# Performance work log

Measured on AMD Instinct MI355X. Metric: run time of the kernel, lower is better.

## Reference

```python
import jax, jax.numpy as jnp
import numpy as np

B, IN_DIM, HID, OUT_DIM, K = 16384, 400, 24, 4096, 64


def setup_inputs() -> dict:
    key = jax.random.key(0)
    ks = jax.random.split(key, 20)
    bnd = 1.0 / np.sqrt(IN_DIM)

    def factorized_eps(k, shape):
        # sign(x)*sqrt(|x|) of small gaussian noise, outer-product factorized
        if len(shape) == 2:
            ko, ki = jax.random.split(k)
            eo = jax.random.normal(ko, (shape[0],)) * 0.001
            ei = jax.random.normal(ki, (shape[1],)) * 0.001
            f = lambda v: jnp.sign(v) * jnp.sqrt(jnp.abs(v))
            return jnp.outer(f(eo), f(ei))
        e = jax.random.normal(k, shape) * 0.001
        return jnp.sign(e) * jnp.sqrt(jnp.abs(e))

    sig2 = 0.5 / np.sqrt(HID)
    sig3 = 0.5 / np.sqrt(OUT_DIM)
    bnd24 = 1.0 / np.sqrt(HID)
    return {
        "x": jax.random.normal(ks[0], (B, IN_DIM), dtype=jnp.float32),
        "possible_moves": jax.random.randint(ks[1], (B, K), 0, OUT_DIM),
        "W1": jax.random.uniform(ks[2], (HID, IN_DIM), minval=-bnd, maxval=bnd),
        "b1": jax.random.uniform(ks[3], (HID,), minval=-bnd, maxval=bnd),
        "mu_w2": jax.random.uniform(ks[4], (HID, HID), minval=-bnd24, maxval=bnd24),
        "mu_b2": jax.random.uniform(ks[5], (HID,), minval=-bnd24, maxval=bnd24),
        "sigma_w2": jnp.full((HID, HID), sig2, dtype=jnp.float32),
        "sigma_b2": jnp.full((HID,), sig2, dtype=jnp.float32),
        "eps_w2": factorized_eps(ks[6], (HID, HID)),
        "eps_b2": factorized_eps(ks[7], (HID,)),
        "mu_w3": jax.random.uniform(ks[8], (OUT_DIM, HID), minval=-bnd24, maxval=bnd24),
        "mu_b3": jax.random.uniform(ks[9], (OUT_DIM,), minval=-bnd24, maxval=bnd24),
        "sigma_w3": jnp.full((OUT_DIM, HID), sig3, dtype=jnp.float32),
        "sigma_b3": jnp.full((OUT_DIM,), sig3, dtype=jnp.float32),
        "eps_w3": factorized_eps(ks[10], (OUT_DIM, HID)),
        "eps_b3": factorized_eps(ks[11], (OUT_DIM,)),
    }


def reference(x, possible_moves, W1, b1, mu_w2, mu_b2, sigma_w2, sigma_b2,
              eps_w2, eps_b2, mu_w3, mu_b3, sigma_w3, sigma_b3, eps_w3, eps_b3):
    h = jax.nn.relu(x @ W1.T + b1)
    w2 = mu_w2 + sigma_w2 * eps_w2
    h = jax.nn.relu(h @ w2.T + (mu_b2 + sigma_b2 * eps_b2))
    w3 = mu_w3 + sigma_w3 * eps_w3
    logits = h @ w3.T + (mu_b3 + sigma_b3 * eps_b3)  # [B, OUT_DIM]
    # scatter 1.0 at legal-move indices per row (vectorized LegalSoftmax)
    rows = jnp.arange(logits.shape[0])[:, None]
    mask = jnp.zeros(logits.shape, logits.dtype).at[rows, possible_moves].set(1.0)
    filtered = logits * mask
    return jnp.where(filtered == 0, -jnp.inf, filtered)
```

## Files before the change

### kernel.cpp

```cpp
#include <hip/hip_runtime.h>
#include <math.h>

#define BATCH 16384
#define IN_DIM 400
#define HID 24
#define OUT_DIM 4096
#define KMOV 64

#define SENT_BITS 0xFF7F0000u

#define WS_W3   0
#define WS_B3   (WS_W3 + OUT_DIM * HID)
#define WS_W2   (WS_B3 + OUT_DIM)
#define WS_B2   (WS_W2 + HID * HID)
#define WS_NEED ((size_t)(WS_B2 + HID) * sizeof(float))

__global__ __launch_bounds__(256) void precompute_folds(
    const float* __restrict__ mu_w2, const float* __restrict__ mu_b2,
    const float* __restrict__ sigma_w2, const float* __restrict__ sigma_b2,
    const float* __restrict__ eps_w2, const float* __restrict__ eps_b2,
    const float* __restrict__ mu_w3, const float* __restrict__ sigma_w3,
    const float* __restrict__ eps_w3, const float* __restrict__ mu_b3,
    const float* __restrict__ sigma_b3, const float* __restrict__ eps_b3,
    float* __restrict__ ws) {
    const int stride = gridDim.x * blockDim.x;
    const int g = blockIdx.x * blockDim.x + threadIdx.x;
    for (int i = g; i < OUT_DIM * HID; i += stride)
        ws[WS_W3 + i] = mu_w3[i] + sigma_w3[i] * eps_w3[i];
    for (int i = g; i < OUT_DIM; i += stride)
        ws[WS_B3 + i] = mu_b3[i] + sigma_b3[i] * eps_b3[i];
    for (int i = g; i < HID * HID; i += stride)
        ws[WS_W2 + i] = mu_w2[i] + sigma_w2[i] * eps_w2[i];
    for (int i = g; i < HID; i += stride)
        ws[WS_B2 + i] = mu_b2[i] + sigma_b2[i] * eps_b2[i];
}

__global__ __launch_bounds__(256) void noisy_onepass(
    const float* __restrict__ x, const int* __restrict__ moves,
    const float* __restrict__ W1, const float* __restrict__ b1,
    const float* __restrict__ ws, float* __restrict__ out) {
    __shared__ float rowbuf[OUT_DIM];
    __shared__ float w2s[HID * HID];
    __shared__ float b2s[HID];
    __shared__ float h1s[HID];
    __shared__ float h2s[HID];

    const int tid = threadIdx.x;
    const int lane = tid & 63;
    const int wave = tid >> 6;
    const int row = blockIdx.x;
    const float SENT = __uint_as_float(SENT_BITS);

    const float4 n4 = make_float4(SENT, SENT, SENT, SENT);
    float4* rb4 = (float4*)rowbuf;
#pragma unroll
    for (int i = 0; i < 4; ++i) rb4[i * 256 + tid] = n4;

    int idx = 0;
    if (tid < KMOV) idx = moves[(size_t)row * KMOV + tid];

    for (int i = tid; i < HID * HID; i += 256) w2s[i] = ws[WS_W2 + i];
    if (tid < HID) b2s[tid] = ws[WS_B2 + tid];

    {
        const float4* xv = (const float4*)(x + (size_t)row * IN_DIM);
        const float4* w1v = (const float4*)W1;
        float4 xa = xv[lane];
        float4 xb = make_float4(0.f, 0.f, 0.f, 0.f);
        const bool hasB = (lane < IN_DIM / 4 - 64);
        if (hasB) xb = xv[64 + lane];

#pragma unroll
        for (int t = 0; t < 6; ++t) {
            const int u = wave * 6 + t;
            const float4* wrow = w1v + u * (IN_DIM / 4);
            float4 wa = wrow[lane];
            float acc = xa.x * wa.x + xa.y * wa.y + xa.z * wa.z + xa.w * wa.w;
            if (hasB) {
                float4 wb = wrow[64 + lane];
                acc += xb.x * wb.x + xb.y * wb.y + xb.z * wb.z + xb.w * wb.w;
            }
            acc += __shfl_xor(acc, 32);
            acc += __shfl_xor(acc, 16);
            acc += __shfl_xor(acc, 8);
            acc += __shfl_xor(acc, 4);
            acc += __shfl_xor(acc, 2);
            acc += __shfl_xor(acc, 1);
            if (lane == 0) h1s[u] = fmaxf(acc + b1[u], 0.f);
        }
    }
    __syncthreads();

    if (tid < HID) {
        float acc = b2s[tid];
#pragma unroll
        for (int j = 0; j < HID; ++j) acc += h1s[j] * w2s[tid * HID + j];
        h2s[tid] = fmaxf(acc, 0.f);
    }
    __syncthreads();

    if (tid < KMOV) {
        float acc = ws[WS_B3 + idx];
        const float4* wr = (const float4*)(ws + WS_W3 + idx * HID);
#pragma unroll
        for (int q = 0; q < 6; ++q) {
            float4 w4 = wr[q];
            acc += h2s[q * 4 + 0] * w4.x + h2s[q * 4 + 1] * w4.y +
                   h2s[q * 4 + 2] * w4.z + h2s[q * 4 + 3] * w4.w;
        }
        rowbuf[idx] = (acc != 0.f) ? acc : SENT;
    }
    __syncthreads();

    float4* orow = (float4*)(out + (size_t)row * OUT_DIM);
#pragma unroll
    for (int i = 0; i < 4; ++i) orow[i * 256 + tid] = rb4[i * 256 + tid];
}

__global__ __launch_bounds__(256) void noisy_fused_fly(
    const float* __restrict__ x, const int* __restrict__ moves,
    const float* __restrict__ W1, const float* __restrict__ b1,
    const float* __restrict__ mu_w2, const float* __restrict__ mu_b2,
    const float* __restrict__ sigma_w2, const float* __restrict__ sigma_b2,
    const float* __restrict__ eps_w2, const float* __restrict__ eps_b2,
    const float* __restrict__ mu_w3, const float* __restrict__ mu_b3,
    const float* __restrict__ sigma_w3, const float* __restrict__ sigma_b3,
    const float* __restrict__ eps_w3, const float* __restrict__ eps_b3,
    float* __restrict__ out) {
    __shared__ float rowbuf[OUT_DIM];
    __shared__ float w2s[HID * HID];
    __shared__ float b2s[HID];
    __shared__ float h1s[HID];
    __shared__ float h2s[HID];

    const int tid = threadIdx.x;
    const int lane = tid & 63;
    const int wave = tid >> 6;
    const int row = blockIdx.x;
    const float SENT = __uint_as_float(SENT_BITS);

    const float4 n4 = make_float4(SENT, SENT, SENT, SENT);
    float4* rb4 = (float4*)rowbuf;
#pragma unroll
    for (int i = 0; i < 4; ++i) rb4[i * 256 + tid] = n4;

    int idx = 0;
    if (tid < KMOV) idx = moves[(size_t)row * KMOV + tid];

    for (int i = tid; i < HID * HID; i += 256)
        w2s[i] = mu_w2[i] + sigma_w2[i] * eps_w2[i];
    if (tid < HID) b2s[tid] = mu_b2[tid] + sigma_b2[tid] * eps_b2[tid];

    {
        const float4* xv = (const float4*)(x + (size_t)row * IN_DIM);
        const float4* w1v = (const float4*)W1;
        float4 xa = xv[lane];
        float4 xb = make_float4(0.f, 0.f, 0.f, 0.f);
        const bool hasB = (lane < IN_DIM / 4 - 64);
        if (hasB) xb = xv[64 + lane];
#pragma unroll
        for (int t = 0; t < 6; ++t) {
            const int u = wave * 6 + t;
            const float4* wrow = w1v + u * (IN_DIM / 4);
            float4 wa = wrow[lane];
            float acc = xa.x * wa.x + xa.y * wa.y + xa.z * wa.z + xa.w * wa.w;
            if (hasB) {
                float4 wb = wrow[64 + lane];
                acc += xb.x * wb.x + xb.y * wb.y + xb.z * wb.z + xb.w * wb.w;
            }
            acc += __shfl_xor(acc, 32);
            acc += __shfl_xor(acc, 16);
            acc += __shfl_xor(acc, 8);
            acc += __shfl_xor(acc, 4);
            acc += __shfl_xor(acc, 2);
            acc += __shfl_xor(acc, 1);
            if (lane == 0) h1s[u] = fmaxf(acc + b1[u], 0.f);
        }
    }
    __syncthreads();

    if (tid < HID) {
        float acc = b2s[tid];
#pragma unroll
        for (int j = 0; j < HID; ++j) acc += h1s[j] * w2s[tid * HID + j];
        h2s[tid] = fmaxf(acc, 0.f);
    }
    __syncthreads();

    if (tid < KMOV) {
        float acc = mu_b3[idx] + sigma_b3[idx] * eps_b3[idx];
        const float4* mr = (const float4*)(mu_w3 + idx * HID);
        const float4* sr = (const float4*)(sigma_w3 + idx * HID);
        const float4* er = (const float4*)(eps_w3 + idx * HID);
#pragma unroll
        for (int q = 0; q < 6; ++q) {
            float4 m4 = mr[q], s4 = sr[q], e4 = er[q];
            acc += h2s[q * 4 + 0] * (m4.x + s4.x * e4.x) +
                   h2s[q * 4 + 1] * (m4.y + s4.y * e4.y) +
                   h2s[q * 4 + 2] * (m4.z + s4.z * e4.z) +
                   h2s[q * 4 + 3] * (m4.w + s4.w * e4.w);
        }
        rowbuf[idx] = (acc != 0.f) ? acc : SENT;
    }
    __syncthreads();

    float4* orow = (float4*)(out + (size_t)row * OUT_DIM);
#pragma unroll
    for (int i = 0; i < 4; ++i) orow[i * 256 + tid] = rb4[i * 256 + tid];
}

extern "C" void kernel_launch(void* const* d_in, const int* in_sizes, int n_in,
                              void* d_out, int out_size, void* d_ws, size_t ws_size,
                              hipStream_t stream) {
    const float* x        = (const float*)d_in[0];
    const int*   moves    = (const int*)d_in[1];
    const float* W1       = (const float*)d_in[2];
    const float* b1       = (const float*)d_in[3];
    const float* mu_w2    = (const float*)d_in[4];
    const float* mu_b2    = (const float*)d_in[5];
    const float* sigma_w2 = (const float*)d_in[6];
    const float* sigma_b2 = (const float*)d_in[7];
    const float* eps_w2   = (const float*)d_in[8];
    const float* eps_b2   = (const float*)d_in[9];
    const float* mu_w3    = (const float*)d_in[10];
    const float* mu_b3    = (const float*)d_in[11];
    const float* sigma_w3 = (const float*)d_in[12];
    const float* sigma_b3 = (const float*)d_in[13];
    const float* eps_w3   = (const float*)d_in[14];
    const float* eps_b3   = (const float*)d_in[15];
    float* out = (float*)d_out;
    float* ws  = (float*)d_ws;

    if (ws_size >= WS_NEED) {
        precompute_folds<<<256, 256, 0, stream>>>(
            mu_w2, mu_b2, sigma_w2, sigma_b2, eps_w2, eps_b2,
            mu_w3, sigma_w3, eps_w3, mu_b3, sigma_b3, eps_b3, ws);
        noisy_onepass<<<BATCH, 256, 0, stream>>>(x, moves, W1, b1, ws, out);
    } else {
        noisy_fused_fly<<<BATCH, 256, 0, stream>>>(
            x, moves, W1, b1, mu_w2, mu_b2, sigma_w2, sigma_b2, eps_w2, eps_b2,
            mu_w3, mu_b3, sigma_w3, sigma_b3, eps_w3, eps_b3, out);
    }
}
```

Baseline: 370.1 us.

## Map one wavefront per batch row and write output directly without LDS staging

Replaces the one-block-per-row kernel with a kernel that gives each 64-lane wavefront a whole row, four rows per block. All three layers are computed in registers with shuffles, removing the shared-memory row buffer and the block-wide barriers. The sentinel fill is written straight to global memory, and an explicit vmcnt wait is placed before the scattered logit stores so they land after the fill. This cuts LDS traffic and synchronisation. In exchange each wave does four times the layer-1 reductions serially, and correctness depends on the wait ordering the fill stores ahead of the scattered stores to the same lines.

```diff
diff --git a/kernel.cpp b/kernel.cpp
--- a/kernel.cpp
+++ b/kernel.cpp
@@ -35,86 +35,76 @@
         ws[WS_B2 + i] = mu_b2[i] + sigma_b2[i] * eps_b2[i];
 }
 
-__global__ __launch_bounds__(256) void noisy_onepass(
+__global__ __launch_bounds__(256) void noisy_waverow(
     const float* __restrict__ x, const int* __restrict__ moves,
     const float* __restrict__ W1, const float* __restrict__ b1,
     const float* __restrict__ ws, float* __restrict__ out) {
-    __shared__ float rowbuf[OUT_DIM];
-    __shared__ float w2s[HID * HID];
-    __shared__ float b2s[HID];
-    __shared__ float h1s[HID];
-    __shared__ float h2s[HID];
-
     const int tid = threadIdx.x;
     const int lane = tid & 63;
-    const int wave = tid >> 6;
-    const int row = blockIdx.x;
+    const int row = (blockIdx.x * 256 + tid) >> 6;
     const float SENT = __uint_as_float(SENT_BITS);
-
     const float4 n4 = make_float4(SENT, SENT, SENT, SENT);
-    float4* rb4 = (float4*)rowbuf;
-#pragma unroll
-    for (int i = 0; i < 4; ++i) rb4[i * 256 + tid] = n4;
-
-    int idx = 0;
-    if (tid < KMOV) idx = moves[(size_t)row * KMOV + tid];
-
-    for (int i = tid; i < HID * HID; i += 256) w2s[i] = ws[WS_W2 + i];
-    if (tid < HID) b2s[tid] = ws[WS_B2 + tid];
-
-    {
-        const float4* xv = (const float4*)(x + (size_t)row * IN_DIM);
-        const float4* w1v = (const float4*)W1;
-        float4 xa = xv[lane];
-        float4 xb = make_float4(0.f, 0.f, 0.f, 0.f);
-        const bool hasB = (lane < IN_DIM / 4 - 64);
-        if (hasB) xb = xv[64 + lane];
-
-#pragma unroll
-        for (int t = 0; t < 6; ++t) {
-            const int u = wave * 6 + t;
-            const float4* wrow = w1v + u * (IN_DIM / 4);
-            float4 wa = wrow[lane];
-            float acc = xa.x * wa.x + xa.y * wa.y + xa.z * wa.z + xa.w * wa.w;
-            if (hasB) {
-                float4 wb = wrow[64 + lane];
-                acc += xb.x * wb.x + xb.y * wb.y + xb.z * wb.z + xb.w * wb.w;
-            }
-            acc += __shfl_xor(acc, 32);
-            acc += __shfl_xor(acc, 16);
-            acc += __shfl_xor(acc, 8);
-            acc += __shfl_xor(acc, 4);
-            acc += __shfl_xor(acc, 2);
-            acc += __shfl_xor(acc, 1);
-            if (lane == 0) h1s[u] = fmaxf(acc + b1[u], 0.f);
-        }
-    }
-    __syncthreads();
-
-    if (tid < HID) {
-        float acc = b2s[tid];
-#pragma unroll
-        for (int j = 0; j < HID; ++j) acc += h1s[j] * w2s[tid * HID + j];
-        h2s[tid] = fmaxf(acc, 0.f);
-    }
-    __syncthreads();
-
-    if (tid < KMOV) {
-        float acc = ws[WS_B3 + idx];
-        const float4* wr = (const float4*)(ws + WS_W3 + idx * HID);
+
+    const int idx = moves[(size_t)row * KMOV + lane];
+
+    const float4* xv = (const float4*)(x + (size_t)row * IN_DIM);
+    float4 xa = xv[lane];
+    float4 xb = make_float4(0.f, 0.f, 0.f, 0.f);
+    const bool hasB = (lane < IN_DIM / 4 - 64);
+    if (hasB) xb = xv[64 + lane];
+
+    float4* orow = (float4*)(out + (size_t)row * OUT_DIM);
+#pragma unroll
+    for (int i = 0; i < 16; ++i) orow[i * 64 + lane] = n4;
+
+    const float4* w1v = (const float4*)W1;
+    float h1[HID];
+#pragma unroll
+    for (int u = 0; u < HID; ++u) {
+        const float4* wrow = w1v + u * (IN_DIM / 4);
+        float4 wa = wrow[lane];
+        float acc = xa.x * wa.x + xa.y * wa.y + xa.z * wa.z + xa.w * wa.w;
+        if (hasB) {
+            float4 wb = wrow[64 + lane];
+            acc += xb.x * wb.x + xb.y * wb.y + xb.z * wb.z + xb.w * wb.w;
+        }
+        acc += __shfl_xor(acc, 32);
+        acc += __shfl_xor(acc, 16);
+        acc += __shfl_xor(acc, 8);
+        acc += __shfl_xor(acc, 4);
+        acc += __shfl_xor(acc, 2);
+        acc += __shfl_xor(acc, 1);
+        h1[u] = fmaxf(acc + b1[u], 0.f);
+    }
+
+    float h2own = 0.f;
+    if (lane < HID) {
+        float acc = ws[WS_B2 + lane];
+        const float4* w2r = (const float4*)(ws + WS_W2 + lane * HID);
 #pragma unroll
         for (int q = 0; q < 6; ++q) {
-            float4 w4 = wr[q];
-            acc += h2s[q * 4 + 0] * w4.x + h2s[q * 4 + 1] * w4.y +
-                   h2s[q * 4 + 2] * w4.z + h2s[q * 4 + 3] * w4.w;
-        }
-        rowbuf[idx] = (acc != 0.f) ? acc : SENT;
-    }
-    __syncthreads();
-
-    float4* orow = (float4*)(out + (size_t)row * OUT_DIM);
-#pragma unroll
-    for (int i = 0; i < 4; ++i) orow[i * 256 + tid] = rb4[i * 256 + tid];
+            float4 w4 = w2r[q];
+            acc += h1[q * 4 + 0] * w4.x + h1[q * 4 + 1] * w4.y +
+                   h1[q * 4 + 2] * w4.z + h1[q * 4 + 3] * w4.w;
+        }
+        h2own = fmaxf(acc, 0.f);
+    }
+    float h2[HID];
+#pragma unroll
+    for (int j = 0; j < HID; ++j) h2[j] = __shfl(h2own, j);
+
+    float acc = ws[WS_B3 + idx];
+    const float4* wr = (const float4*)(ws + WS_W3 + idx * HID);
+#pragma unroll
+    for (int q = 0; q < 6; ++q) {
+        float4 w4 = wr[q];
+        acc += h2[q * 4 + 0] * w4.x + h2[q * 4 + 1] * w4.y +
+               h2[q * 4 + 2] * w4.z + h2[q * 4 + 3] * w4.w;
+    }
+    float val = (acc != 0.f) ? acc : SENT;
+
+    asm volatile("s_waitcnt vmcnt(0)" ::: "memory");
+    out[(size_t)row * OUT_DIM + idx] = val;
 }
 
 __global__ __launch_bounds__(256) void noisy_fused_fly(
@@ -235,7 +225,7 @@
         precompute_folds<<<256, 256, 0, stream>>>(
             mu_w2, mu_b2, sigma_w2, sigma_b2, eps_w2, eps_b2,
             mu_w3, sigma_w3, eps_w3, mu_b3, sigma_b3, eps_b3, ws);
-        noisy_onepass<<<BATCH, 256, 0, stream>>>(x, moves, W1, b1, ws, out);
+        noisy_waverow<<<BATCH / 4, 256, 0, stream>>>(x, moves, W1, b1, ws, out);
     } else {
         noisy_fused_fly<<<BATCH, 256, 0, stream>>>(
             x, moves, W1, b1, mu_w2, mu_b2, sigma_w2, sigma_b2, eps_w2, eps_b2,
```

Result: slower. 412.1 us (+11.3%).
